# Optimization experiments

Hardware: AMD Instinct MI355X
Metric: run time of the kernel (lower is better)

The kernel has to match this reference:

```python
import jax, jax.numpy as jnp
import numpy as np

GAMMA = 0.9865


def setup_inputs() -> dict:
    key = jax.random.key(0)
    ks = jax.random.split(key, 6)
    B, T, DIN, D = 8, 2048, 1024, 1024
    return {
        "xq": jax.random.normal(ks[0], (B, T, DIN), dtype=jnp.float32),
        "xk": jax.random.normal(ks[1], (B, T, DIN), dtype=jnp.float32),
        "xv": jax.random.normal(ks[2], (B, T, DIN), dtype=jnp.float32),
        "Wq": jax.random.normal(ks[3], (DIN, D), dtype=jnp.float32) * (DIN ** -0.5),
        "Wk": jax.random.normal(ks[4], (DIN, D), dtype=jnp.float32) * (DIN ** -0.5),
        "Wv": jax.random.normal(ks[5], (DIN, D), dtype=jnp.float32) * (DIN ** -0.5),
    }


def reference(xq, xk, xv, Wq, Wk, Wv):
    # Dense projections (no bias)
    Q = jnp.einsum("btd,de->bte", xq, Wq)  # [B,T,D]
    K = jnp.einsum("btd,de->bte", xk, Wk)
    V = jnp.einsum("btd,de->bte", xv, Wv)

    # einsum('ib,bj->bj', K_t^T, V_t) == (sum_i K[b,t,i]) * V[b,t,:]
    ksum = jnp.sum(K, axis=-1)            # [B,T]
    u = ksum[..., None] * V               # [B,T,D]
    # recurrence starts at t=1 with s[0]=0, so u[0] never contributes
    u = u * (jnp.arange(u.shape[1]) > 0)[None, :, None]

    def step(s, u_t):
        s = s * jnp.float32(GAMMA) + u_t
        return s, s

    s0 = jnp.zeros(u.shape[::2], dtype=u.dtype)          # [B,D]
    _, S = jax.lax.scan(step, s0, jnp.swapaxes(u, 0, 1))  # S: [T,B,D]
    return Q * jnp.swapaxes(S, 0, 1)                      # [B,T,D]
```

## Files before the change

### kernel.cpp

```cpp
#include <hip/hip_runtime.h>
#include <hip/hip_bf16.h>

#define GAMMA 0.9865f

typedef __attribute__((ext_vector_type(8))) short bf16x8;
typedef __attribute__((ext_vector_type(4))) float f32x4;

static constexpr int Bb  = 8;
static constexpr int Tt  = 2048;
static constexpr int DIN = 1024;
static constexpr int Dd  = 1024;
static constexpr int Mm  = Bb * Tt;
static constexpr int CL  = 64;
static constexpr int NC  = Tt / CL;

__device__ __forceinline__ void gload16(const void* g, void* l) {
  __builtin_amdgcn_global_load_lds(
      (const __attribute__((address_space(1))) void*)g,
      (__attribute__((address_space(3))) void*)l, 16, 0, 0);
}

__global__ void wsum_kernel(const float* __restrict__ Wk, float* __restrict__ wsum) {
  int row  = blockIdx.x * 4 + (threadIdx.x >> 6);
  int lane = threadIdx.x & 63;
  const float4* rp = (const float4*)(Wk + (size_t)row * DIN);
  float s = 0.f;
#pragma unroll
  for (int i = 0; i < 4; ++i) {
    float4 v = rp[lane + i * 64];
    s += v.x + v.y + v.z + v.w;
  }
  for (int off = 32; off; off >>= 1) s += __shfl_down(s, off);
  if (lane == 0) wsum[row] = s;
}

__global__ void wt_kernel(const float* __restrict__ Wq, const float* __restrict__ Wv,
                          __hip_bfloat16* __restrict__ Wt) {
  const float* W = blockIdx.z ? Wv : Wq;
  __hip_bfloat16* outp = Wt + (size_t)blockIdx.z * DIN * Dd;
  __shared__ float tile[32][33];
  int k0 = blockIdx.x * 32, n0 = blockIdx.y * 32;
  int tx = threadIdx.x, ty = threadIdx.y;
#pragma unroll
  for (int i = 0; i < 4; ++i)
    tile[ty + i * 8][tx] = W[(size_t)(k0 + ty + i * 8) * Dd + n0 + tx];
  __syncthreads();
#pragma unroll
  for (int i = 0; i < 4; ++i)
    outp[(size_t)(n0 + ty + i * 8) * DIN + k0 + tx] =
        __float2bfloat16(tile[tx][ty + i * 8]);
}

__global__ void cast_kernel(const float* __restrict__ xq, const float* __restrict__ xv,
                            __hip_bfloat16* __restrict__ oq, __hip_bfloat16* __restrict__ ov) {
  const float* src = blockIdx.y ? xv : xq;
  __hip_bfloat16* dst = blockIdx.y ? ov : oq;
  size_t i = (size_t)blockIdx.x * 256 + threadIdx.x;
  float4 v = ((const float4*)src)[i];
  union { __hip_bfloat16 h[4]; ushort4 u; } cv;
  cv.h[0] = __float2bfloat16(v.x);
  cv.h[1] = __float2bfloat16(v.y);
  cv.h[2] = __float2bfloat16(v.z);
  cv.h[3] = __float2bfloat16(v.w);
  ((ushort4*)dst)[i] = cv.u;
}

__global__ __launch_bounds__(256) void gemm_kernel(
    const __hip_bfloat16* __restrict__ Aq, const __hip_bfloat16* __restrict__ Av,
    const __hip_bfloat16* __restrict__ Wt,
    __hip_bfloat16* __restrict__ Qbf, __hip_bfloat16* __restrict__ Vbf) {
  const int z = blockIdx.z;
  const __hip_bfloat16* Ab = z ? Av : Aq;
  const __hip_bfloat16* Bg = Wt + (size_t)(z * Dd + blockIdx.y * 128) * DIN;
  __hip_bfloat16* Cc = z ? Vbf : Qbf;

  const int m0 = blockIdx.x * 128;
  const int n0 = blockIdx.y * 128;
  const int tid = threadIdx.x;

  __shared__ __align__(16) __hip_bfloat16 As[128 * 32];
  __shared__ __align__(16) __hip_bfloat16 Bs[128 * 32];

  const int wv = tid >> 6, lane = tid & 63;
  const int wm = (wv >> 1) * 64, wn = (wv & 1) * 64;
  const int fq = lane >> 4, fr = lane & 15;

  f32x4 acc[4][4] = {};

  const __hip_bfloat16* Ag = Ab + (size_t)m0 * DIN;

  for (int k0 = 0; k0 < DIN; k0 += 32) {
#pragma unroll
    for (int r = 0; r < 2; ++r) {
      int c = r * 256 + tid;
      int row = c >> 2, kq = (c & 3) << 3;
      gload16(Ag + (size_t)row * DIN + k0 + kq, (char*)As + c * 16);
    }
#pragma unroll
    for (int r = 0; r < 2; ++r) {
      int c = r * 256 + tid;
      int row = c >> 2, kq = (c & 3) << 3;
      gload16(Bg + (size_t)row * DIN + k0 + kq, (char*)Bs + c * 16);
    }
    __syncthreads();

    const bf16x8* Avv = (const bf16x8*)As;
    const bf16x8* Bvv = (const bf16x8*)Bs;
    bf16x8 a[4], b[4];
#pragma unroll
    for (int i = 0; i < 4; ++i) {
      a[i] = Avv[(wm + i * 16 + fr) * 4 + fq];
      b[i] = Bvv[(wn + i * 16 + fr) * 4 + fq];
    }
#pragma unroll
    for (int mi = 0; mi < 4; ++mi)
#pragma unroll
      for (int ni = 0; ni < 4; ++ni)
        acc[mi][ni] = __builtin_amdgcn_mfma_f32_16x16x32_bf16(a[mi], b[ni], acc[mi][ni], 0, 0, 0);
    __syncthreads();
  }

#pragma unroll
  for (int mi = 0; mi < 4; ++mi) {
#pragma unroll
    for (int ni = 0; ni < 4; ++ni) {
      f32x4 v = acc[mi][ni];
      int row = m0 + wm + mi * 16 + fq * 4;
      int col = n0 + wn + ni * 16 + fr;
#pragma unroll
      for (int j = 0; j < 4; ++j)
        Cc[(size_t)(row + j) * Dd + col] = __float2bfloat16(v[j]);
    }
  }
}

__global__ void ksum_kernel(const float* __restrict__ xk, const float* __restrict__ wsum,
                            float* __restrict__ ksum) {
  int row  = blockIdx.x * 4 + (threadIdx.x >> 6);
  int lane = threadIdx.x & 63;
  const float4* rp = (const float4*)(xk + (size_t)row * DIN);
  const float4* wp = (const float4*)wsum;
  float s = 0.f;
#pragma unroll
  for (int i = 0; i < 4; ++i) {
    float4 a = rp[lane + i * 64];
    float4 w = wp[lane + i * 64];
    s += a.x * w.x + a.y * w.y + a.z * w.z + a.w * w.w;
  }
  for (int off = 32; off; off >>= 1) s += __shfl_down(s, off);
  if (lane == 0) ksum[row] = s;
}

__global__ void scanA_kernel(const __hip_bfloat16* __restrict__ Vbf,
                             const float* __restrict__ ksum,
                             float* __restrict__ E) {
  int b = blockIdx.x, c = blockIdx.y;
  int d = blockIdx.z * 256 + threadIdx.x;
  const __hip_bfloat16* Vp = Vbf + ((size_t)(b * Tt + c * CL) * Dd) + d;
  const float* kp = ksum + b * Tt + c * CL;
  float s = 0.f;
#pragma unroll 8
  for (int t = 0; t < CL; ++t) {
    float u = kp[t] * __bfloat162float(Vp[(size_t)t * Dd]);
    if (c == 0 && t == 0) u = 0.f;
    s = s * GAMMA + u;
  }
  E[((size_t)b * NC + c) * Dd + d] = s;
}

__global__ void scanB_kernel(const float* __restrict__ E, float* __restrict__ carry,
                             float gCL) {
  int b = blockIdx.x;
  int d = blockIdx.y * 256 + threadIdx.x;
  float send = 0.f;
  for (int c = 0; c < NC; ++c) {
    size_t idx = ((size_t)b * NC + c) * Dd + d;
    float e = E[idx];
    carry[idx] = send;
    send = e + gCL * send;
  }
}

__global__ void final_kernel(const __hip_bfloat16* __restrict__ Vbf,
                             const __hip_bfloat16* __restrict__ Qbf,
                             const float* __restrict__ ksum,
                             const float* __restrict__ carry,
                             float* __restrict__ outp) {
  int b = blockIdx.x, c = blockIdx.y;
  int d = blockIdx.z * 256 + threadIdx.x;
  size_t base = ((size_t)(b * Tt + c * CL) * Dd) + d;
  float s = carry[((size_t)b * NC + c) * Dd + d];
  const float* kp = ksum + b * Tt + c * CL;
#pragma unroll 4
  for (int t = 0; t < CL; ++t) {
    float u = kp[t] * __bfloat162float(Vbf[base + (size_t)t * Dd]);
    if (c == 0 && t == 0) u = 0.f;
    s = s * GAMMA + u;
    outp[base + (size_t)t * Dd] = __bfloat162float(Qbf[base + (size_t)t * Dd]) * s;
  }
}

extern "C" void kernel_launch(void* const* d_in, const int* in_sizes, int n_in,
                              void* d_out, int out_size, void* d_ws, size_t ws_size,
                              hipStream_t stream) {
  (void)in_sizes; (void)n_in; (void)out_size; (void)ws_size;
  const float* xq = (const float*)d_in[0];
  const float* xk = (const float*)d_in[1];
  const float* xv = (const float*)d_in[2];
  const float* Wq = (const float*)d_in[3];
  const float* Wk = (const float*)d_in[4];
  const float* Wv = (const float*)d_in[5];
  float* outp = (float*)d_out;

  char* ws = (char*)d_ws;
  size_t off = 0;
  auto alloc = [&](size_t bytes) {
    char* p = ws + off;
    off += (bytes + 255) & ~(size_t)255;
    return p;
  };
  __hip_bfloat16* xq_bf = (__hip_bfloat16*)alloc((size_t)Mm * DIN * 2);
  __hip_bfloat16* xv_bf = (__hip_bfloat16*)alloc((size_t)Mm * DIN * 2);
  __hip_bfloat16* Wt    = (__hip_bfloat16*)alloc((size_t)2 * DIN * Dd * 2);
  __hip_bfloat16* Qbf   = (__hip_bfloat16*)alloc((size_t)Mm * Dd * 2);
  __hip_bfloat16* Vbf   = (__hip_bfloat16*)alloc((size_t)Mm * Dd * 2);
  float* wsum  = (float*)alloc((size_t)DIN * 4);
  float* ksum  = (float*)alloc((size_t)Mm * 4);
  float* E     = (float*)alloc((size_t)Bb * NC * Dd * 4);
  float* carry = (float*)alloc((size_t)Bb * NC * Dd * 4);

  double g = 1.0;
  for (int i = 0; i < CL; ++i) g *= (double)GAMMA;
  float gCL = (float)g;

  wsum_kernel<<<DIN / 4, 256, 0, stream>>>(Wk, wsum);
  wt_kernel<<<dim3(DIN / 32, Dd / 32, 2), dim3(32, 8), 0, stream>>>(Wq, Wv, Wt);
  cast_kernel<<<dim3(Mm * DIN / 4 / 256, 2), 256, 0, stream>>>(xq, xv, xq_bf, xv_bf);
  gemm_kernel<<<dim3(Mm / 128, Dd / 128, 2), 256, 0, stream>>>(xq_bf, xv_bf, Wt, Qbf, Vbf);
  ksum_kernel<<<Mm / 4, 256, 0, stream>>>(xk, wsum, ksum);
  scanA_kernel<<<dim3(Bb, NC, Dd / 256), 256, 0, stream>>>(Vbf, ksum, E);
  scanB_kernel<<<dim3(Bb, Dd / 256), 256, 0, stream>>>(E, carry, gCL);
  final_kernel<<<dim3(Bb, NC, Dd / 256), 256, 0, stream>>>(Vbf, Qbf, ksum, carry, outp);
}
```

Before: 174.1 us.

## Replace GEMM with 256x256 double-buffered 8-wave pipelined MFMA kernel

New measurement: 158.2 us. 1.1x faster.

```diff
diff --git a/kernel.cpp b/kernel.cpp
--- a/kernel.cpp
+++ b/kernel.cpp
@@ -13,11 +13,18 @@
 static constexpr int Mm  = Bb * Tt;
 static constexpr int CL  = 64;
 static constexpr int NC  = Tt / CL;
+static constexpr int NT  = DIN / 64;
 
 __device__ __forceinline__ void gload16(const void* g, void* l) {
   __builtin_amdgcn_global_load_lds(
       (const __attribute__((address_space(1))) void*)g,
       (__attribute__((address_space(3))) void*)l, 16, 0, 0);
+}
+
+__device__ __forceinline__ void bar() {
+  asm volatile("" ::: "memory");
+  __builtin_amdgcn_s_barrier();
+  asm volatile("" ::: "memory");
 }
 
 __global__ void wsum_kernel(const float* __restrict__ Wk, float* __restrict__ wsum) {
@@ -65,63 +72,124 @@
   ((ushort4*)dst)[i] = cv.u;
 }
 
-__global__ __launch_bounds__(256) void gemm_kernel(
+
+__device__ __forceinline__ void stage_half(const __hip_bfloat16* g, char* l, int tid) {
+#pragma unroll
+  for (int j = 0; j < 2; ++j) {
+    int c = tid + j * 512;
+    int row = c >> 3, ch = c & 7;
+    gload16(g + (size_t)row * DIN + ((ch ^ (row & 7)) << 3), l + c * 16);
+  }
+}
+
+__device__ __forceinline__ bf16x8 lds_frag(const char* base, int row, int kc) {
+  return *(const bf16x8*)(base + (((row << 3) + (kc ^ (row & 7))) << 4));
+}
+
+#define MFMA_QUAD(MLO, NLO)                                                  \
+  _Pragma("unroll") for (int mi = 0; mi < 4; ++mi)                           \
+  _Pragma("unroll") for (int ni = 0; ni < 2; ++ni)                           \
+  _Pragma("unroll") for (int ks = 0; ks < 2; ++ks)                           \
+      acc[(MLO) + mi][(NLO) + ni] = __builtin_amdgcn_mfma_f32_16x16x32_bf16( \
+          a[(MLO) + mi][ks], b[(NLO) + ni][ks], acc[(MLO) + mi][(NLO) + ni], 0, 0, 0);
+
+__global__ __launch_bounds__(512, 2) void gemm8_kernel(
     const __hip_bfloat16* __restrict__ Aq, const __hip_bfloat16* __restrict__ Av,
     const __hip_bfloat16* __restrict__ Wt,
     __hip_bfloat16* __restrict__ Qbf, __hip_bfloat16* __restrict__ Vbf) {
-  const int z = blockIdx.z;
+  extern __shared__ char lds[];
+
+  int lin = blockIdx.x;
+  int wg  = (lin & 7) * 64 + (lin >> 3);
+  int z   = wg >> 8, rem = wg & 255;
+  int by  = rem & 3, bx = rem >> 2;
+
   const __hip_bfloat16* Ab = z ? Av : Aq;
-  const __hip_bfloat16* Bg = Wt + (size_t)(z * Dd + blockIdx.y * 128) * DIN;
+  const int m0 = bx * 256, n0 = by * 256;
+  const __hip_bfloat16* Ag = Ab + (size_t)m0 * DIN;
+  const __hip_bfloat16* Bg = Wt + ((size_t)z * Dd + n0) * DIN;
   __hip_bfloat16* Cc = z ? Vbf : Qbf;
 
-  const int m0 = blockIdx.x * 128;
-  const int n0 = blockIdx.y * 128;
   const int tid = threadIdx.x;
-
-  __shared__ __align__(16) __hip_bfloat16 As[128 * 32];
-  __shared__ __align__(16) __hip_bfloat16 Bs[128 * 32];
-
   const int wv = tid >> 6, lane = tid & 63;
-  const int wm = (wv >> 1) * 64, wn = (wv & 1) * 64;
+  const int wm = (wv >> 2) * 128, wn = (wv & 3) * 64;
   const int fq = lane >> 4, fr = lane & 15;
 
-  f32x4 acc[4][4] = {};
-
-  const __hip_bfloat16* Ag = Ab + (size_t)m0 * DIN;
-
-  for (int k0 = 0; k0 < DIN; k0 += 32) {
-#pragma unroll
-    for (int r = 0; r < 2; ++r) {
-      int c = r * 256 + tid;
-      int row = c >> 2, kq = (c & 3) << 3;
-      gload16(Ag + (size_t)row * DIN + k0 + kq, (char*)As + c * 16);
+  f32x4 acc[8][4] = {};
+
+  stage_half(Ag,                  lds,                 tid);
+  stage_half(Ag + 128 * DIN,      lds + 16384,         tid);
+  stage_half(Bg,                  lds + 32768,         tid);
+  stage_half(Bg + 128 * DIN,      lds + 49152,         tid);
+  stage_half(Ag + 64,             lds + 65536,         tid);
+  stage_half(Ag + 128 * DIN + 64, lds + 65536 + 16384, tid);
+  asm volatile("s_waitcnt vmcnt(4)" ::: "memory");
+  bar();
+
+  for (int t = 0; t < NT; ++t) {
+    char* buf  = lds + (t & 1) * 65536;
+    char* bufN = lds + ((t + 1) & 1) * 65536;
+    const char* At = buf;
+    const char* Bt = buf + 32768;
+    bf16x8 a[8][2], b[4][2];
+
+#pragma unroll
+    for (int mi = 0; mi < 4; ++mi)
+#pragma unroll
+      for (int ks = 0; ks < 2; ++ks)
+        a[mi][ks] = lds_frag(At, wm + mi * 16 + fr, ks * 4 + fq);
+#pragma unroll
+    for (int ni = 0; ni < 2; ++ni)
+#pragma unroll
+      for (int ks = 0; ks < 2; ++ks)
+        b[ni][ks] = lds_frag(Bt, wn + ni * 16 + fr, ks * 4 + fq);
+    if (t + 1 < NT) stage_half(Bg + (size_t)(t + 1) * 64, bufN + 32768, tid);
+    bar();
+    __builtin_amdgcn_s_setprio(1);
+    MFMA_QUAD(0, 0);
+    __builtin_amdgcn_s_setprio(0);
+    bar();
+
+#pragma unroll
+    for (int mi = 4; mi < 8; ++mi)
+#pragma unroll
+      for (int ks = 0; ks < 2; ++ks)
+        a[mi][ks] = lds_frag(At, wm + mi * 16 + fr, ks * 4 + fq);
+    if (t + 1 < NT)
+      stage_half(Bg + 128 * DIN + (size_t)(t + 1) * 64, bufN + 49152, tid);
+    bar();
+    __builtin_amdgcn_s_setprio(1);
+    MFMA_QUAD(4, 0);
+    __builtin_amdgcn_s_setprio(0);
+    bar();
+
+#pragma unroll
+    for (int ni = 2; ni < 4; ++ni)
+#pragma unroll
+      for (int ks = 0; ks < 2; ++ks)
+        b[ni][ks] = lds_frag(Bt, wn + ni * 16 + fr, ks * 4 + fq);
+    if (t + 2 < NT) stage_half(Ag + (size_t)(t + 2) * 64, buf, tid);
+    bar();
+    __builtin_amdgcn_s_setprio(1);
+    MFMA_QUAD(0, 2);
+    __builtin_amdgcn_s_setprio(0);
+    bar();
+
+    if (t + 2 < NT)
+      stage_half(Ag + 128 * DIN + (size_t)(t + 2) * 64, buf + 16384, tid);
+    if (t + 1 < NT) {
+      if (t + 2 < NT) asm volatile("s_waitcnt vmcnt(4)" ::: "memory");
+      else            asm volatile("s_waitcnt vmcnt(0)" ::: "memory");
     }
-#pragma unroll
-    for (int r = 0; r < 2; ++r) {
-      int c = r * 256 + tid;
-      int row = c >> 2, kq = (c & 3) << 3;
-      gload16(Bg + (size_t)row * DIN + k0 + kq, (char*)Bs + c * 16);
-    }
-    __syncthreads();
-
-    const bf16x8* Avv = (const bf16x8*)As;
-    const bf16x8* Bvv = (const bf16x8*)Bs;
-    bf16x8 a[4], b[4];
-#pragma unroll
-    for (int i = 0; i < 4; ++i) {
-      a[i] = Avv[(wm + i * 16 + fr) * 4 + fq];
-      b[i] = Bvv[(wn + i * 16 + fr) * 4 + fq];
-    }
-#pragma unroll
-    for (int mi = 0; mi < 4; ++mi)
-#pragma unroll
-      for (int ni = 0; ni < 4; ++ni)
-        acc[mi][ni] = __builtin_amdgcn_mfma_f32_16x16x32_bf16(a[mi], b[ni], acc[mi][ni], 0, 0, 0);
-    __syncthreads();
-  }
-
-#pragma unroll
-  for (int mi = 0; mi < 4; ++mi) {
+    bar();
+    __builtin_amdgcn_s_setprio(1);
+    MFMA_QUAD(4, 2);
+    __builtin_amdgcn_s_setprio(0);
+    bar();
+  }
+
+#pragma unroll
+  for (int mi = 0; mi < 8; ++mi) {
 #pragma unroll
     for (int ni = 0; ni < 4; ++ni) {
       f32x4 v = acc[mi][ni];
@@ -233,10 +301,13 @@
   for (int i = 0; i < CL; ++i) g *= (double)GAMMA;
   float gCL = (float)g;
 
+  (void)hipFuncSetAttribute((const void*)gemm8_kernel,
+                            hipFuncAttributeMaxDynamicSharedMemorySize, 131072);
+
   wsum_kernel<<<DIN / 4, 256, 0, stream>>>(Wk, wsum);
   wt_kernel<<<dim3(DIN / 32, Dd / 32, 2), dim3(32, 8), 0, stream>>>(Wq, Wv, Wt);
   cast_kernel<<<dim3(Mm * DIN / 4 / 256, 2), 256, 0, stream>>>(xq, xv, xq_bf, xv_bf);
-  gemm_kernel<<<dim3(Mm / 128, Dd / 128, 2), 256, 0, stream>>>(xq_bf, xv_bf, Wt, Qbf, Vbf);
+  gemm8_kernel<<<512, 512, 131072, stream>>>(xq_bf, xv_bf, Wt, Qbf, Vbf);
   ksum_kernel<<<Mm / 4, 256, 0, stream>>>(xk, wsum, ksum);
   scanA_kernel<<<dim3(Bb, NC, Dd / 256), 256, 0, stream>>>(Vbf, ksum, E);
   scanB_kernel<<<dim3(Bb, Dd / 256), 256, 0, stream>>>(E, carry, gCL);
```
